# Optimization experiments

Hardware: AMD Instinct MI355X
Metric: run time of the kernel (lower is better)

Reference implementation:

```python
import jax, jax.numpy as jnp
import numpy as np

LN_EPS = 1e-6  # flax nn.LayerNorm default epsilon
NEG_SLOPE = 0.01  # jax.nn.leaky_relu default


def _layer_norm(x, scale, bias):
    m = jnp.mean(x, axis=-1, keepdims=True)
    v = jnp.mean(jnp.square(x - m), axis=-1, keepdims=True)
    return (x - m) * jax.lax.rsqrt(v + LN_EPS) * scale + bias


def setup_inputs() -> dict:
    key = jax.random.key(0)
    ks = jax.random.split(key, 10)
    B, D1, D2, OUT = 32768, 1024, 512, 1024
    inp = {
        "x1": jax.random.normal(ks[0], (B, D1), dtype=jnp.float32),
        "x2": jax.random.normal(ks[1], (B, D2), dtype=jnp.float32),
        # LayerNorm params (one per stream)
        "ln_scale1": jnp.ones((D1,), jnp.float32),
        "ln_bias1": jnp.zeros((D1,), jnp.float32),
        "ln_scale2": jnp.ones((D2,), jnp.float32),
        "ln_bias2": jnp.zeros((D2,), jnp.float32),
        # output Dense per stream: Dense(output_size)
        "W_out1": jax.random.normal(ks[2], (D1, OUT), jnp.float32) / np.sqrt(D1),
        "b_out1": jnp.zeros((OUT,), jnp.float32),
        "W_out2": jax.random.normal(ks[3], (D2, OUT), jnp.float32) / np.sqrt(D2),
        "b_out2": jnp.zeros((OUT,), jnp.float32),
        # gate Dense per stream: Dense(gate_size=output_size) for POINTWISE
        "W_g1": jax.random.normal(ks[4], (D1, OUT), jnp.float32) / np.sqrt(D1),
        "b_g1": jnp.zeros((OUT,), jnp.float32),
        "W_g2": jax.random.normal(ks[5], (D2, OUT), jnp.float32) / np.sqrt(D2),
        "b_g2": jnp.zeros((OUT,), jnp.float32),
    }
    return inp


def reference(x1, x2, ln_scale1, ln_bias1, ln_scale2, ln_bias2,
              W_out1, b_out1, W_out2, b_out2,
              W_g1, b_g1, W_g2, b_g2):
    # per-stream: LayerNorm -> leaky_relu -> Dense(output_size); pre-Dense
    # activation is also fed to the gate Dense.
    f1 = jax.nn.leaky_relu(_layer_norm(x1, ln_scale1, ln_bias1), NEG_SLOPE)
    f2 = jax.nn.leaky_relu(_layer_norm(x2, ln_scale2, ln_bias2), NEG_SLOPE)
    out1 = f1 @ W_out1 + b_out1  # [B, OUT]
    out2 = f2 @ W_out2 + b_out2  # [B, OUT]
    # two-stream POINTWISE gate: sum of gate Denses, sigmoid; the original
    # broadcasts gate [B,OUT] over stack([out1,out2]) and sums axis 0,
    # i.e. output = gate * (out1 + out2).
    gate = jax.nn.sigmoid((f1 @ W_g1 + b_g1) + (f2 @ W_g2 + b_g2))
    return gate * (out1 + out2)
```

## Files before the change

### kernel.cpp

```cpp
#include <hip/hip_runtime.h>
#include <hip/hip_bf16.h>
#include <stdint.h>

typedef __bf16 bf16x8 __attribute__((ext_vector_type(8)));
typedef float floatx4 __attribute__((ext_vector_type(4)));

__device__ __forceinline__ ushort f2bf(float f) {
  union { float f; uint32_t u; } v; v.f = f;
  uint32_t r = (v.u + 0x7fffu + ((v.u >> 16) & 1u)) >> 16;
  return (ushort)r;
}

__device__ __forceinline__ void load_lds16(const ushort* g, ushort* l) {
  __builtin_amdgcn_global_load_lds(
      (__attribute__((address_space(1))) void*)g,
      (__attribute__((address_space(3))) void*)l, 16, 0, 0);
}

__device__ __forceinline__ float leaky(float x) { return x >= 0.f ? x : 0.01f * x; }

__global__ __launch_bounds__(256) void ln2_kernel(
    const float* __restrict__ x1, const float* __restrict__ x2,
    const float* __restrict__ sc1p, const float* __restrict__ bi1p,
    const float* __restrict__ sc2p, const float* __restrict__ bi2p,
    ushort* __restrict__ f) {
  const int row = (blockIdx.x << 2) + (threadIdx.x >> 6);
  const int lane = threadIdx.x & 63;
  const float4* X1 = (const float4*)(x1 + (size_t)row * 1024);
  const float4* X2 = (const float4*)(x2 + (size_t)row * 512);
  float4 v1[4], v2[2];
#pragma unroll
  for (int j = 0; j < 4; j++) v1[j] = X1[j * 64 + lane];
#pragma unroll
  for (int j = 0; j < 2; j++) v2[j] = X2[j * 64 + lane];
  float s1 = 0.f, q1 = 0.f, s2 = 0.f, q2 = 0.f;
#pragma unroll
  for (int j = 0; j < 4; j++) {
    s1 += v1[j].x + v1[j].y + v1[j].z + v1[j].w;
    q1 += v1[j].x * v1[j].x + v1[j].y * v1[j].y + v1[j].z * v1[j].z + v1[j].w * v1[j].w;
  }
#pragma unroll
  for (int j = 0; j < 2; j++) {
    s2 += v2[j].x + v2[j].y + v2[j].z + v2[j].w;
    q2 += v2[j].x * v2[j].x + v2[j].y * v2[j].y + v2[j].z * v2[j].z + v2[j].w * v2[j].w;
  }
#pragma unroll
  for (int o = 1; o < 64; o <<= 1) {
    s1 += __shfl_xor(s1, o);
    q1 += __shfl_xor(q1, o);
    s2 += __shfl_xor(s2, o);
    q2 += __shfl_xor(q2, o);
  }
  const float m1 = s1 * (1.0f / 1024.0f);
  const float r1 = rsqrtf(q1 * (1.0f / 1024.0f) - m1 * m1 + 1e-6f);
  const float m2 = s2 * (1.0f / 512.0f);
  const float r2 = rsqrtf(q2 * (1.0f / 512.0f) - m2 * m2 + 1e-6f);
  ushort* frow = f + (size_t)row * 1536;
#pragma unroll
  for (int j = 0; j < 4; j++) {
    const float4 sc = ((const float4*)sc1p)[j * 64 + lane];
    const float4 bi = ((const float4*)bi1p)[j * 64 + lane];
    const float y0 = leaky((v1[j].x - m1) * r1 * sc.x + bi.x);
    const float y1 = leaky((v1[j].y - m1) * r1 * sc.y + bi.y);
    const float y2 = leaky((v1[j].z - m1) * r1 * sc.z + bi.z);
    const float y3 = leaky((v1[j].w - m1) * r1 * sc.w + bi.w);
    ushort4 o; o.x = f2bf(y0); o.y = f2bf(y1); o.z = f2bf(y2); o.w = f2bf(y3);
    ((ushort4*)frow)[j * 64 + lane] = o;
  }
#pragma unroll
  for (int j = 0; j < 2; j++) {
    const float4 sc = ((const float4*)sc2p)[j * 64 + lane];
    const float4 bi = ((const float4*)bi2p)[j * 64 + lane];
    const float z0 = leaky((v2[j].x - m2) * r2 * sc.x + bi.x);
    const float z1 = leaky((v2[j].y - m2) * r2 * sc.y + bi.y);
    const float z2 = leaky((v2[j].z - m2) * r2 * sc.z + bi.z);
    const float z3 = leaky((v2[j].w - m2) * r2 * sc.w + bi.w);
    ushort4 o; o.x = f2bf(z0); o.y = f2bf(z1); o.z = f2bf(z2); o.w = f2bf(z3);
    ((ushort4*)(frow + 1024))[j * 64 + lane] = o;
  }
}

__global__ __launch_bounds__(256) void wprep_kernel(
    const float* __restrict__ Wo1, const float* __restrict__ Wo2,
    const float* __restrict__ Wg1, const float* __restrict__ Wg2,
    ushort* __restrict__ WT) {
  __shared__ float tile[32][33];
  const int k0 = blockIdx.x * 32;
  const int j0 = blockIdx.y * 32;
  const int s = blockIdx.z;
  const float* Wa = s ? Wg1 : Wo1;
  const float* Wb = s ? Wg2 : Wo2;
  const int tx = threadIdx.x;
  const int ty = threadIdx.y;
#pragma unroll
  for (int r = 0; r < 4; r++) {
    const int k = k0 + ty + 8 * r;
    const float val = (k < 1024) ? Wa[(size_t)k * 1024 + j0 + tx]
                                 : Wb[(size_t)(k - 1024) * 1024 + j0 + tx];
    tile[ty + 8 * r][tx] = val;
  }
  __syncthreads();
#pragma unroll
  for (int r = 0; r < 4; r++) {
    const int j = j0 + ty + 8 * r;
    const int c = j & 63;
    const int n = (j >> 6) * 128 + (c >> 5) * 64 + s * 32 + ((c >> 4) & 1) * 16 + (c & 15);
    WT[(size_t)n * 1536 + k0 + tx] = f2bf(tile[tx][ty + 8 * r]);
  }
}

__global__ __launch_bounds__(512, 2) void gemm_fused(
    const ushort* __restrict__ A,
    const ushort* __restrict__ Bt,
    const float* __restrict__ bo1, const float* __restrict__ bo2,
    const float* __restrict__ bg1, const float* __restrict__ bg2,
    float* __restrict__ out) {
  __shared__ __align__(16) ushort As[2][16384];
  __shared__ __align__(16) ushort Bs[2][16384];
  const int orig = blockIdx.x;
  const int swz = (orig & 7) * 128 + (orig >> 3);
  const int mt = swz >> 3;
  const int nt = swz & 7;
  const int tid = threadIdx.x;
  const int wave = tid >> 6, lane = tid & 63;
  const int wr = wave >> 2, wcol = wave & 3;
  const int low = lane & 15, quad = lane >> 4;

  const int srow = wave * 8 + (lane >> 3);
  const int schunk = (lane & 7) ^ (lane >> 3);
  const ushort* gA0 = A + ((size_t)mt * 256 + srow) * 1536 + schunk * 8;
  const ushort* gB0 = Bt + ((size_t)nt * 256 + srow) * 1536 + schunk * 8;

  const int q2 = quad ^ (low & 3);
  const int kx = (low >> 2) & 1;
  const int offA_k0 = (wr * 128 + low) * 64 + (q2 + 4 * kx) * 8;
  const int offA_k1 = (wr * 128 + low) * 64 + (q2 + 4 * (1 - kx)) * 8;
  const int offB_k0 = (wcol * 64 + low) * 64 + (q2 + 4 * kx) * 8;
  const int offB_k1 = (wcol * 64 + low) * 64 + (q2 + 4 * (1 - kx)) * 8;

  floatx4 acc[8][4];
#pragma unroll
  for (int m = 0; m < 8; m++)
#pragma unroll
    for (int n = 0; n < 4; n++) acc[m][n] = (floatx4)0.0f;

#define STAGE_A(BUF, KT) do { \
    const ushort* s_ = gA0 + (KT) * 64; \
    ushort* d_ = &As[BUF][wave * 512]; \
    load_lds16(s_, d_); \
    load_lds16(s_ + 64 * 1536, d_ + 4096); \
    load_lds16(s_ + 128 * 1536, d_ + 8192); \
    load_lds16(s_ + 192 * 1536, d_ + 12288); \
  } while (0)
#define STAGE_B(BUF, KT) do { \
    const ushort* s_ = gB0 + (KT) * 64; \
    ushort* d_ = &Bs[BUF][wave * 512]; \
    load_lds16(s_, d_); \
    load_lds16(s_ + 64 * 1536, d_ + 4096); \
    load_lds16(s_ + 128 * 1536, d_ + 8192); \
    load_lds16(s_ + 192 * 1536, d_ + 12288); \
  } while (0)

  STAGE_A(0, 0);
  STAGE_B(0, 0);
  asm volatile("s_waitcnt vmcnt(0)" ::: "memory");
  __builtin_amdgcn_s_barrier();
  asm volatile("" ::: "memory");

#define TILE_STEP(CUR, T) do { \
    const ushort* Ac = &As[CUR][0]; \
    const ushort* Bc = &Bs[CUR][0]; \
    const bool pf = (T) < 23; \
    bf16x8 a[4], b[4]; \
     \
    _Pragma("unroll") for (int m = 0; m < 4; m++) a[m] = *(const bf16x8*)(Ac + offA_k0 + m * 1024); \
    _Pragma("unroll") for (int n = 0; n < 4; n++) b[n] = *(const bf16x8*)(Bc + offB_k0 + n * 1024); \
    if (pf) STAGE_A((CUR) ^ 1, (T) + 1); \
    asm volatile("" ::: "memory"); \
    __builtin_amdgcn_s_barrier(); \
    __builtin_amdgcn_s_setprio(1); \
    _Pragma("unroll") for (int m = 0; m < 4; m++) \
      _Pragma("unroll") for (int n = 0; n < 4; n++) \
        acc[m][n] = __builtin_amdgcn_mfma_f32_16x16x32_bf16(a[m], b[n], acc[m][n], 0, 0, 0); \
    __builtin_amdgcn_s_setprio(0); \
    asm volatile("" ::: "memory"); \
    __builtin_amdgcn_s_barrier(); \
     \
    _Pragma("unroll") for (int m = 0; m < 4; m++) a[m] = *(const bf16x8*)(Ac + offA_k0 + (m + 4) * 1024); \
    if (pf) STAGE_B((CUR) ^ 1, (T) + 1); \
    asm volatile("" ::: "memory"); \
    __builtin_amdgcn_s_barrier(); \
    __builtin_amdgcn_s_setprio(1); \
    _Pragma("unroll") for (int m = 0; m < 4; m++) \
      _Pragma("unroll") for (int n = 0; n < 4; n++) \
        acc[m + 4][n] = __builtin_amdgcn_mfma_f32_16x16x32_bf16(a[m], b[n], acc[m + 4][n], 0, 0, 0); \
    __builtin_amdgcn_s_setprio(0); \
    asm volatile("" ::: "memory"); \
    __builtin_amdgcn_s_barrier(); \
     \
    _Pragma("unroll") for (int m = 0; m < 4; m++) a[m] = *(const bf16x8*)(Ac + offA_k1 + m * 1024); \
    _Pragma("unroll") for (int n = 0; n < 4; n++) b[n] = *(const bf16x8*)(Bc + offB_k1 + n * 1024); \
    asm volatile("" ::: "memory"); \
    __builtin_amdgcn_s_barrier(); \
    __builtin_amdgcn_s_setprio(1); \
    _Pragma("unroll") for (int m = 0; m < 4; m++) \
      _Pragma("unroll") for (int n = 0; n < 4; n++) \
        acc[m][n] = __builtin_amdgcn_mfma_f32_16x16x32_bf16(a[m], b[n], acc[m][n], 0, 0, 0); \
    __builtin_amdgcn_s_setprio(0); \
    asm volatile("" ::: "memory"); \
    __builtin_amdgcn_s_barrier(); \
     \
    _Pragma("unroll") for (int m = 0; m < 4; m++) a[m] = *(const bf16x8*)(Ac + offA_k1 + (m + 4) * 1024); \
    asm volatile("" ::: "memory"); \
    __builtin_amdgcn_s_barrier(); \
    __builtin_amdgcn_s_setprio(1); \
    _Pragma("unroll") for (int m = 0; m < 4; m++) \
      _Pragma("unroll") for (int n = 0; n < 4; n++) \
        acc[m + 4][n] = __builtin_amdgcn_mfma_f32_16x16x32_bf16(a[m], b[n], acc[m + 4][n], 0, 0, 0); \
    __builtin_amdgcn_s_setprio(0); \
    asm volatile("s_waitcnt vmcnt(0)" ::: "memory"); \
    __builtin_amdgcn_s_barrier(); \
    asm volatile("" ::: "memory"); \
  } while (0)

  for (int tt = 0; tt < 12; tt++) {
    TILE_STEP(0, 2 * tt);
    TILE_STEP(1, 2 * tt + 1);
  }
#undef TILE_STEP
#undef STAGE_A
#undef STAGE_B

  const int colbase = (nt * 4 + wcol) << 5;
#pragma unroll
  for (int n = 0; n < 2; n++) {
    const int col = colbase + n * 16 + low;
    const float bs = bo1[col] + bo2[col];
    const float bg = bg1[col] + bg2[col];
#pragma unroll
    for (int m = 0; m < 8; m++) {
      const floatx4 S = acc[m][n];
      const floatx4 G = acc[m][n + 2];
      const size_t rb = (size_t)mt * 256 + wr * 128 + m * 16 + quad * 4;
#pragma unroll
      for (int r = 0; r < 4; r++) {
        const float sv = S[r] + bs;
        const float gv = G[r] + bg;
        const float gate = 1.0f / (1.0f + __expf(-gv));
        out[(rb + r) * 1024 + col] = gate * sv;
      }
    }
  }
}

extern "C" void kernel_launch(void* const* d_in, const int* in_sizes, int n_in,
                              void* d_out, int out_size, void* d_ws, size_t ws_size,
                              hipStream_t stream) {
  const float* x1 = (const float*)d_in[0];
  const float* x2 = (const float*)d_in[1];
  const float* ln_s1 = (const float*)d_in[2];
  const float* ln_b1 = (const float*)d_in[3];
  const float* ln_s2 = (const float*)d_in[4];
  const float* ln_b2 = (const float*)d_in[5];
  const float* W_out1 = (const float*)d_in[6];
  const float* b_out1 = (const float*)d_in[7];
  const float* W_out2 = (const float*)d_in[8];
  const float* b_out2 = (const float*)d_in[9];
  const float* W_g1 = (const float*)d_in[10];
  const float* b_g1 = (const float*)d_in[11];
  const float* W_g2 = (const float*)d_in[12];
  const float* b_g2 = (const float*)d_in[13];
  float* out = (float*)d_out;

  ushort* f = (ushort*)d_ws;
  ushort* WT = f + (size_t)32768 * 1536;

  ln2_kernel<<<8192, 256, 0, stream>>>(x1, x2, ln_s1, ln_b1, ln_s2, ln_b2, f);
  wprep_kernel<<<dim3(48, 32, 2), dim3(32, 8), 0, stream>>>(W_out1, W_out2, W_g1, W_g2, WT);
  gemm_fused<<<dim3(1024), dim3(512), 0, stream>>>(f, WT, b_out1, b_out2, b_g1, b_g2, out);
}
```

Baseline: 517.2 us.

## Split A-tile prefetch by k-half and relax vmcnt waits in GEMM main loop

Result: slower. 539.1 us (+4.2%).

```diff
diff --git a/kernel.cpp b/kernel.cpp
--- a/kernel.cpp
+++ b/kernel.cpp
@@ -144,92 +144,156 @@
 #pragma unroll
     for (int n = 0; n < 4; n++) acc[m][n] = (floatx4)0.0f;
 
-#define STAGE_A(BUF, KT) do { \
-    const ushort* s_ = gA0 + (KT) * 64; \
-    ushort* d_ = &As[BUF][wave * 512]; \
-    load_lds16(s_, d_); \
-    load_lds16(s_ + 64 * 1536, d_ + 4096); \
-    load_lds16(s_ + 128 * 1536, d_ + 8192); \
-    load_lds16(s_ + 192 * 1536, d_ + 12288); \
-  } while (0)
-#define STAGE_B(BUF, KT) do { \
-    const ushort* s_ = gB0 + (KT) * 64; \
-    ushort* d_ = &Bs[BUF][wave * 512]; \
-    load_lds16(s_, d_); \
-    load_lds16(s_ + 64 * 1536, d_ + 4096); \
-    load_lds16(s_ + 128 * 1536, d_ + 8192); \
-    load_lds16(s_ + 192 * 1536, d_ + 12288); \
-  } while (0)
-
-  STAGE_A(0, 0);
-  STAGE_B(0, 0);
-  asm volatile("s_waitcnt vmcnt(0)" ::: "memory");
+  {
+    ushort* dA = &As[0][wave * 512];
+    ushort* dB = &Bs[0][wave * 512];
+    load_lds16(gB0, dB);
+    load_lds16(gB0 + 64 * 1536, dB + 4096);
+    load_lds16(gB0 + 128 * 1536, dB + 8192);
+    load_lds16(gB0 + 192 * 1536, dB + 12288);
+    load_lds16(gA0, dA);
+    load_lds16(gA0 + 128 * 1536, dA + 8192);
+    load_lds16(gA0 + 64 * 1536, dA + 4096);
+    load_lds16(gA0 + 192 * 1536, dA + 12288);
+  }
+  asm volatile("s_waitcnt vmcnt(2)" ::: "memory");
   __builtin_amdgcn_s_barrier();
   asm volatile("" ::: "memory");
 
-#define TILE_STEP(CUR, T) do { \
-    const ushort* Ac = &As[CUR][0]; \
-    const ushort* Bc = &Bs[CUR][0]; \
-    const bool pf = (T) < 23; \
-    bf16x8 a[4], b[4]; \
-     \
-    _Pragma("unroll") for (int m = 0; m < 4; m++) a[m] = *(const bf16x8*)(Ac + offA_k0 + m * 1024); \
-    _Pragma("unroll") for (int n = 0; n < 4; n++) b[n] = *(const bf16x8*)(Bc + offB_k0 + n * 1024); \
-    if (pf) STAGE_A((CUR) ^ 1, (T) + 1); \
-    asm volatile("" ::: "memory"); \
-    __builtin_amdgcn_s_barrier(); \
-    __builtin_amdgcn_s_setprio(1); \
-    _Pragma("unroll") for (int m = 0; m < 4; m++) \
-      _Pragma("unroll") for (int n = 0; n < 4; n++) \
-        acc[m][n] = __builtin_amdgcn_mfma_f32_16x16x32_bf16(a[m], b[n], acc[m][n], 0, 0, 0); \
-    __builtin_amdgcn_s_setprio(0); \
-    asm volatile("" ::: "memory"); \
-    __builtin_amdgcn_s_barrier(); \
-     \
-    _Pragma("unroll") for (int m = 0; m < 4; m++) a[m] = *(const bf16x8*)(Ac + offA_k0 + (m + 4) * 1024); \
-    if (pf) STAGE_B((CUR) ^ 1, (T) + 1); \
-    asm volatile("" ::: "memory"); \
-    __builtin_amdgcn_s_barrier(); \
-    __builtin_amdgcn_s_setprio(1); \
-    _Pragma("unroll") for (int m = 0; m < 4; m++) \
-      _Pragma("unroll") for (int n = 0; n < 4; n++) \
-        acc[m + 4][n] = __builtin_amdgcn_mfma_f32_16x16x32_bf16(a[m], b[n], acc[m + 4][n], 0, 0, 0); \
-    __builtin_amdgcn_s_setprio(0); \
-    asm volatile("" ::: "memory"); \
-    __builtin_amdgcn_s_barrier(); \
-     \
-    _Pragma("unroll") for (int m = 0; m < 4; m++) a[m] = *(const bf16x8*)(Ac + offA_k1 + m * 1024); \
-    _Pragma("unroll") for (int n = 0; n < 4; n++) b[n] = *(const bf16x8*)(Bc + offB_k1 + n * 1024); \
-    asm volatile("" ::: "memory"); \
-    __builtin_amdgcn_s_barrier(); \
-    __builtin_amdgcn_s_setprio(1); \
-    _Pragma("unroll") for (int m = 0; m < 4; m++) \
-      _Pragma("unroll") for (int n = 0; n < 4; n++) \
-        acc[m][n] = __builtin_amdgcn_mfma_f32_16x16x32_bf16(a[m], b[n], acc[m][n], 0, 0, 0); \
-    __builtin_amdgcn_s_setprio(0); \
-    asm volatile("" ::: "memory"); \
-    __builtin_amdgcn_s_barrier(); \
-     \
-    _Pragma("unroll") for (int m = 0; m < 4; m++) a[m] = *(const bf16x8*)(Ac + offA_k1 + (m + 4) * 1024); \
-    asm volatile("" ::: "memory"); \
-    __builtin_amdgcn_s_barrier(); \
-    __builtin_amdgcn_s_setprio(1); \
-    _Pragma("unroll") for (int m = 0; m < 4; m++) \
-      _Pragma("unroll") for (int n = 0; n < 4; n++) \
-        acc[m + 4][n] = __builtin_amdgcn_mfma_f32_16x16x32_bf16(a[m], b[n], acc[m + 4][n], 0, 0, 0); \
-    __builtin_amdgcn_s_setprio(0); \
-    asm volatile("s_waitcnt vmcnt(0)" ::: "memory"); \
-    __builtin_amdgcn_s_barrier(); \
-    asm volatile("" ::: "memory"); \
-  } while (0)
-
-  for (int tt = 0; tt < 12; tt++) {
-    TILE_STEP(0, 2 * tt);
-    TILE_STEP(1, 2 * tt + 1);
-  }
-#undef TILE_STEP
-#undef STAGE_A
-#undef STAGE_B
+  for (int t = 0; t < 23; ++t) {
+    const int cur = t & 1;
+    const ushort* Ac = (const ushort*)As + cur * 16384;
+    const ushort* Bc = (const ushort*)Bs + cur * 16384;
+    ushort* dA = (ushort*)As + (cur ^ 1) * 16384 + wave * 512;
+    ushort* dB = (ushort*)Bs + (cur ^ 1) * 16384 + wave * 512;
+    const ushort* sA = gA0 + (t + 1) * 64;
+    const ushort* sB = gB0 + (t + 1) * 64;
+    bf16x8 a[4], b[4];
+#pragma unroll
+    for (int m = 0; m < 4; m++) a[m] = *(const bf16x8*)(Ac + offA_k0 + m * 1024);
+#pragma unroll
+    for (int n = 0; n < 4; n++) b[n] = *(const bf16x8*)(Bc + offB_k0 + n * 1024);
+    load_lds16(sB, dB);
+    load_lds16(sB + 64 * 1536, dB + 4096);
+    load_lds16(sB + 128 * 1536, dB + 8192);
+    load_lds16(sB + 192 * 1536, dB + 12288);
+    asm volatile("" ::: "memory");
+    __builtin_amdgcn_s_barrier();
+    __builtin_amdgcn_s_setprio(1);
+#pragma unroll
+    for (int m = 0; m < 4; m++)
+#pragma unroll
+      for (int n = 0; n < 4; n++)
+        acc[m][n] = __builtin_amdgcn_mfma_f32_16x16x32_bf16(a[m], b[n], acc[m][n], 0, 0, 0);
+    __builtin_amdgcn_s_setprio(0);
+    asm volatile("s_waitcnt vmcnt(4)" ::: "memory");
+    __builtin_amdgcn_s_barrier();
+#pragma unroll
+    for (int m = 0; m < 4; m++) a[m] = *(const bf16x8*)(Ac + offA_k0 + (m + 4) * 1024);
+    load_lds16(sA, dA);
+    load_lds16(sA + 128 * 1536, dA + 8192);
+    asm volatile("" ::: "memory");
+    __builtin_amdgcn_s_barrier();
+    __builtin_amdgcn_s_setprio(1);
+#pragma unroll
+    for (int m = 0; m < 4; m++)
+#pragma unroll
+      for (int n = 0; n < 4; n++)
+        acc[m + 4][n] = __builtin_amdgcn_mfma_f32_16x16x32_bf16(a[m], b[n], acc[m + 4][n], 0, 0, 0);
+    __builtin_amdgcn_s_setprio(0);
+    asm volatile("" ::: "memory");
+    __builtin_amdgcn_s_barrier();
+#pragma unroll
+    for (int m = 0; m < 4; m++) a[m] = *(const bf16x8*)(Ac + offA_k1 + m * 1024);
+#pragma unroll
+    for (int n = 0; n < 4; n++) b[n] = *(const bf16x8*)(Bc + offB_k1 + n * 1024);
+    load_lds16(sA + 64 * 1536, dA + 4096);
+    load_lds16(sA + 192 * 1536, dA + 12288);
+    asm volatile("" ::: "memory");
+    __builtin_amdgcn_s_barrier();
+    __builtin_amdgcn_s_setprio(1);
+#pragma unroll
+    for (int m = 0; m < 4; m++)
+#pragma unroll
+      for (int n = 0; n < 4; n++)
+        acc[m][n] = __builtin_amdgcn_mfma_f32_16x16x32_bf16(a[m], b[n], acc[m][n], 0, 0, 0);
+    __builtin_amdgcn_s_setprio(0);
+    asm volatile("" ::: "memory");
+    __builtin_amdgcn_s_barrier();
+#pragma unroll
+    for (int m = 0; m < 4; m++) a[m] = *(const bf16x8*)(Ac + offA_k1 + (m + 4) * 1024);
+    asm volatile("" ::: "memory");
+    __builtin_amdgcn_s_barrier();
+    __builtin_amdgcn_s_setprio(1);
+#pragma unroll
+    for (int m = 0; m < 4; m++)
+#pragma unroll
+      for (int n = 0; n < 4; n++)
+        acc[m + 4][n] = __builtin_amdgcn_mfma_f32_16x16x32_bf16(a[m], b[n], acc[m + 4][n], 0, 0, 0);
+    __builtin_amdgcn_s_setprio(0);
+    asm volatile("s_waitcnt vmcnt(2)" ::: "memory");
+    __builtin_amdgcn_s_barrier();
+    asm volatile("" ::: "memory");
+  }
+
+  {
+    const ushort* Ac = (const ushort*)As + 16384;
+    const ushort* Bc = (const ushort*)Bs + 16384;
+    bf16x8 a[4], b[4];
+#pragma unroll
+    for (int m = 0; m < 4; m++) a[m] = *(const bf16x8*)(Ac + offA_k0 + m * 1024);
+#pragma unroll
+    for (int n = 0; n < 4; n++) b[n] = *(const bf16x8*)(Bc + offB_k0 + n * 1024);
+    asm volatile("" ::: "memory");
+    __builtin_amdgcn_s_barrier();
+    __builtin_amdgcn_s_setprio(1);
+#pragma unroll
+    for (int m = 0; m < 4; m++)
+#pragma unroll
+      for (int n = 0; n < 4; n++)
+        acc[m][n] = __builtin_amdgcn_mfma_f32_16x16x32_bf16(a[m], b[n], acc[m][n], 0, 0, 0);
+    __builtin_amdgcn_s_setprio(0);
+    asm volatile("s_waitcnt vmcnt(0)" ::: "memory");
+    __builtin_amdgcn_s_barrier();
+#pragma unroll
+    for (int m = 0; m < 4; m++) a[m] = *(const bf16x8*)(Ac + offA_k0 + (m + 4) * 1024);
+    asm volatile("" ::: "memory");
+    __builtin_amdgcn_s_barrier();
+    __builtin_amdgcn_s_setprio(1);
+#pragma unroll
+    for (int m = 0; m < 4; m++)
+#pragma unroll
+      for (int n = 0; n < 4; n++)
+        acc[m + 4][n] = __builtin_amdgcn_mfma_f32_16x16x32_bf16(a[m], b[n], acc[m + 4][n], 0, 0, 0);
+    __builtin_amdgcn_s_setprio(0);
+    asm volatile("" ::: "memory");
+    __builtin_amdgcn_s_barrier();
+#pragma unroll
+    for (int m = 0; m < 4; m++) a[m] = *(const bf16x8*)(Ac + offA_k1 + m * 1024);
+#pragma unroll
+    for (int n = 0; n < 4; n++) b[n] = *(const bf16x8*)(Bc + offB_k1 + n * 1024);
+    asm volatile("" ::: "memory");
+    __builtin_amdgcn_s_barrier();
+    __builtin_amdgcn_s_setprio(1);
+#pragma unroll
+    for (int m = 0; m < 4; m++)
+#pragma unroll
+      for (int n = 0; n < 4; n++)
+        acc[m][n] = __builtin_amdgcn_mfma_f32_16x16x32_bf16(a[m], b[n], acc[m][n], 0, 0, 0);
+    __builtin_amdgcn_s_setprio(0);
+    asm volatile("" ::: "memory");
+    __builtin_amdgcn_s_barrier();
+#pragma unroll
+    for (int m = 0; m < 4; m++) a[m] = *(const bf16x8*)(Ac + offA_k1 + (m + 4) * 1024);
+    asm volatile("" ::: "memory");
+    __builtin_amdgcn_s_setprio(1);
+#pragma unroll
+    for (int m = 0; m < 4; m++)
+#pragma unroll
+      for (int n = 0; n < 4; n++)
+        acc[m + 4][n] = __builtin_amdgcn_mfma_f32_16x16x32_bf16(a[m], b[n], acc[m + 4][n], 0, 0, 0);
+    __builtin_amdgcn_s_setprio(0);
+  }
 
   const int colbase = (nt * 4 + wcol) << 5;
 #pragma unroll
```
